# Kernel tuning notes

Hardware: AMD Instinct MI355X
Metric: run time of the kernel (lower is better)

Reference implementation:

```python
import jax, jax.numpy as jnp
import numpy as np


def setup_inputs() -> dict:
    key = jax.random.key(0)
    k1, k2, k3 = jax.random.split(key, 3)
    B, L, D, OUT = 4, 256, 768, 256
    text = jax.random.normal(k1, (B, L, D), dtype=jnp.float32)
    weight = jax.random.normal(k2, (OUT, 2 * D), dtype=jnp.float32) * (1.0 / np.sqrt(2 * D))
    bias = jax.random.normal(k3, (OUT,), dtype=jnp.float32) * 0.02
    return {"text": text, "weight": weight, "bias": bias}


def reference(text, weight, bias):
    # torch: hidden_1[b,i,j,:] = text[b,j,:]; hidden_2[b,i,j,:] = text[b,i,:]
    # cat((hidden_1, hidden_2), -1) @ weight.T + bias
    # Algebraically: out[b,i,j] = text[b,j] @ W1.T + text[b,i] @ W2.T + bias
    D = text.shape[-1]
    w1 = weight[:, :D]   # multiplies hidden_1 (the j-indexed part)
    w2 = weight[:, D:]   # multiplies hidden_2 (the i-indexed part)
    pj = jnp.einsum('bjd,od->bjo', text, w1)  # [B, L, out]
    pi = jnp.einsum('bid,od->bio', text, w2)  # [B, L, out]
    out = pi[:, :, None, :] + pj[:, None, :, :] + bias  # [B, L, L, out]
    return out
```

## Files before the change

kernel.cpp:

```cpp
#include <hip/hip_runtime.h>


#define DDIM 768
#define WT_FLOATS (768 * 512)
#define P_HALF (1024 * 256)

typedef float f4 __attribute__((ext_vector_type(4)));

__global__ __launch_bounds__(256) void k_transpose(const float* __restrict__ W,
                                                   float* __restrict__ WT) {
    __shared__ float t[32][33];
    const int c0 = blockIdx.x * 32;
    const int o0 = blockIdx.y * 32;
    const int tx = threadIdx.x & 31, ty = threadIdx.x >> 5;
#pragma unroll
    for (int yy = ty; yy < 32; yy += 8)
        t[yy][tx] = W[(size_t)(o0 + yy) * 1536 + c0 + tx];
    __syncthreads();
#pragma unroll
    for (int yy = ty; yy < 32; yy += 8) {
        int c = c0 + yy;
        int h = (c >= 768) ? 1 : 0;
        int d = c - h * 768;
        WT[(size_t)d * 512 + h * 256 + o0 + tx] = t[tx][yy];
    }
}

__global__ __launch_bounds__(1024) void k_gemv(const float* __restrict__ text,
                                               const float* __restrict__ bias,
                                               const float* __restrict__ WT,
                                               float* __restrict__ P) {
    __shared__ float red[4][4][256];
    const int m0 = blockIdx.x * 4;
    const int h  = blockIdx.y;
    const int o  = threadIdx.x & 255;
    const int dg = __builtin_amdgcn_readfirstlane(threadIdx.x >> 8);
    float acc[4];
#pragma unroll
    for (int r = 0; r < 4; ++r) acc[r] = 0.0f;
    const float* t0 = text + (size_t)m0 * DDIM + dg * 192;
    const float* wt = WT + (size_t)(dg * 192) * 512 + h * 256 + o;
#pragma unroll 8
    for (int d = 0; d < 192; ++d) {
        float w = wt[(size_t)d * 512];
#pragma unroll
        for (int r = 0; r < 4; ++r)
            acc[r] = fmaf(t0[(size_t)r * DDIM + d], w, acc[r]);
    }
#pragma unroll
    for (int r = 0; r < 4; ++r) red[dg][r][o] = acc[r];
    __syncthreads();
    {
        int r = threadIdx.x >> 8, oo = threadIdx.x & 255;
        float s = red[0][r][oo] + red[1][r][oo] + red[2][r][oo] + red[3][r][oo];
        if (h) s += bias[oo];
        P[(size_t)h * P_HALF + (size_t)(m0 + r) * 256 + oo] = s;
    }
}

__global__ __launch_bounds__(256) void k_bcast(const float* __restrict__ P,
                                               float* __restrict__ out) {
    const int bid  = blockIdx.x;
    const int r    = bid >> 1;
    const int half = bid & 1;
    const int b    = r >> 8;
    const int o4 = (threadIdx.x & 63) * 4;
    const int jg = threadIdx.x >> 6;
    const f4 pi4 = *(const f4*)(P + (size_t)P_HALF + (size_t)r * 256 + o4);
    const float* pjb = P + (size_t)b * 65536;
    float* outr = out + (size_t)r * 65536;
    const int j0 = half * 128 + jg;
#pragma unroll 8
    for (int j = j0; j < j0 + 128 - jg; j += 4) {
        f4 pj4 = *(const f4*)(pjb + j * 256 + o4);
        f4 v = pi4 + pj4;
        *(f4*)(outr + j * 256 + o4) = v;
    }
}

extern "C" void kernel_launch(void* const* d_in, const int* in_sizes, int n_in,
                              void* d_out, int out_size, void* d_ws, size_t ws_size,
                              hipStream_t stream) {
    const float* text   = (const float*)d_in[0];
    const float* weight = (const float*)d_in[1];
    const float* bias   = (const float*)d_in[2];
    float* out = (float*)d_out;
    float* WT  = (float*)d_ws;
    float* P   = WT + WT_FLOATS;

    k_transpose<<<dim3(48, 8), 256, 0, stream>>>(weight, WT);
    k_gemv<<<dim3(256, 2), 1024, 0, stream>>>(text, bias, WT, P);
    k_bcast<<<2048, 256, 0, stream>>>(P, out);
}
```

Baseline: 69.82 us.

## Restructure projection GEMV to vectorized per-thread outputs without split-D reduction

The projection kernel now gives each thread four output channels for two rows, uses float4 weight loads, and loops over the full hidden dimension. This removes the shared-memory reduction and the barrier. Blocks shrink to 256 threads covering 8 rows each. The trade-off is fewer total threads and a longer serial dependency chain per thread, which may reduce latency hiding.

```diff
diff --git a/kernel.cpp b/kernel.cpp
--- a/kernel.cpp
+++ b/kernel.cpp
@@ -26,36 +26,31 @@
     }
 }
 
-__global__ __launch_bounds__(1024) void k_gemv(const float* __restrict__ text,
-                                               const float* __restrict__ bias,
-                                               const float* __restrict__ WT,
-                                               float* __restrict__ P) {
-    __shared__ float red[4][4][256];
-    const int m0 = blockIdx.x * 4;
-    const int h  = blockIdx.y;
-    const int o  = threadIdx.x & 255;
-    const int dg = __builtin_amdgcn_readfirstlane(threadIdx.x >> 8);
-    float acc[4];
-#pragma unroll
-    for (int r = 0; r < 4; ++r) acc[r] = 0.0f;
-    const float* t0 = text + (size_t)m0 * DDIM + dg * 192;
-    const float* wt = WT + (size_t)(dg * 192) * 512 + h * 256 + o;
+__global__ __launch_bounds__(256) void k_gemv(const float* __restrict__ text,
+                                              const float* __restrict__ bias,
+                                              const float* __restrict__ WT,
+                                              float* __restrict__ P) {
+    const int m0  = blockIdx.x * 8;
+    const int h   = blockIdx.y;
+    const int o64 = threadIdx.x & 63;
+    const int rg  = __builtin_amdgcn_readfirstlane(threadIdx.x >> 6);
+    const int r0  = m0 + rg * 2;
+    f4 a0 = (f4)0.0f, a1 = (f4)0.0f;
+    const float* t0 = text + (size_t)r0 * DDIM;
+    const float* wt = WT + h * 256 + o64 * 4;
 #pragma unroll 8
-    for (int d = 0; d < 192; ++d) {
-        float w = wt[(size_t)d * 512];
-#pragma unroll
-        for (int r = 0; r < 4; ++r)
-            acc[r] = fmaf(t0[(size_t)r * DDIM + d], w, acc[r]);
+    for (int d = 0; d < DDIM; ++d) {
+        f4 w4 = *(const f4*)(wt + (size_t)d * 512);
+        a0 += w4 * t0[d];
+        a1 += w4 * t0[DDIM + d];
     }
-#pragma unroll
-    for (int r = 0; r < 4; ++r) red[dg][r][o] = acc[r];
-    __syncthreads();
-    {
-        int r = threadIdx.x >> 8, oo = threadIdx.x & 255;
-        float s = red[0][r][oo] + red[1][r][oo] + red[2][r][oo] + red[3][r][oo];
-        if (h) s += bias[oo];
-        P[(size_t)h * P_HALF + (size_t)(m0 + r) * 256 + oo] = s;
+    if (h) {
+        f4 b = *(const f4*)(bias + o64 * 4);
+        a0 += b; a1 += b;
     }
+    float* p = P + (size_t)h * P_HALF + (size_t)r0 * 256 + o64 * 4;
+    *(f4*)p = a0;
+    *(f4*)(p + 256) = a1;
 }
 
 __global__ __launch_bounds__(256) void k_bcast(const float* __restrict__ P,
@@ -89,6 +84,6 @@
     float* P   = WT + WT_FLOATS;
 
     k_transpose<<<dim3(48, 8), 256, 0, stream>>>(weight, WT);
-    k_gemv<<<dim3(256, 2), 1024, 0, stream>>>(text, bias, WT, P);
+    k_gemv<<<dim3(128, 2), 256, 0, stream>>>(text, bias, WT, P);
     k_bcast<<<2048, 256, 0, stream>>>(P, out);
 }
```

Result: slower. 92.37 us (+32.3%).
